# Performance work log

Measured on AMD Instinct MI355X. Metric: run time of the kernel, lower is better.

The kernel has to match this reference:

```python
import jax, jax.numpy as jnp
import numpy as np


def _add_self_loops(src, dst, n):
    loop = jnp.arange(n, dtype=src.dtype)
    return jnp.concatenate([src, loop]), jnp.concatenate([dst, loop])


def _graph_conv(x, src, dst, n, W, b):
    # DGL GraphConv with norm='both':
    #   h = D_in^{-1/2} * A^T * (D_out^{-1/2} * x) @ W + b
    ones = jnp.ones(src.shape, dtype=x.dtype)
    deg_out = jax.ops.segment_sum(ones, src, num_segments=n)
    deg_in = jax.ops.segment_sum(ones, dst, num_segments=n)
    norm_s = jax.lax.rsqrt(jnp.maximum(deg_out, 1.0))
    norm_d = jax.lax.rsqrt(jnp.maximum(deg_in, 1.0))
    msg = (x * norm_s[:, None])[src]                      # [E, d] gather
    agg = jax.ops.segment_sum(msg, dst, num_segments=n)   # [N, d] scatter-add
    return (agg * norm_d[:, None]) @ W + b


def _ntype_forward(x, src, dst, W0, b0, W1, b1):
    n = x.shape[0]
    src, dst = _add_self_loops(src, dst, n)  # dgl.add_self_loop each layer; graph is static
    h = _graph_conv(x, src, dst, n, W0, b0)
    h = jax.nn.relu(h)  # dropout skipped: eval mode (training=False)
    h = _graph_conv(h, src, dst, n, W1, b1)
    return h


def setup_inputs() -> dict:
    key = jax.random.key(0)
    ks = jax.random.split(key, 16)
    NA, NB, EA, EB = 50000, 30000, 600000, 300000
    DA, DB, H = 256, 128, 128
    s = 0.05
    return {
        "feat_a": jax.random.normal(ks[0], (NA, DA), jnp.float32),
        "feat_b": jax.random.normal(ks[1], (NB, DB), jnp.float32),
        "src_a": jax.random.randint(ks[2], (EA,), 0, NA),
        "dst_a": jax.random.randint(ks[3], (EA,), 0, NA),
        "src_b": jax.random.randint(ks[4], (EB,), 0, NB),
        "dst_b": jax.random.randint(ks[5], (EB,), 0, NB),
        "Wa0": jax.random.normal(ks[6], (DA, H), jnp.float32) * s,
        "ba0": jnp.zeros((H,), jnp.float32),
        "Wa1": jax.random.normal(ks[7], (H, H), jnp.float32) * s,
        "ba1": jnp.zeros((H,), jnp.float32),
        "Wb0": jax.random.normal(ks[8], (DB, H), jnp.float32) * s,
        "bb0": jnp.zeros((H,), jnp.float32),
        "Wb1": jax.random.normal(ks[9], (H, H), jnp.float32) * s,
        "bb1": jnp.zeros((H,), jnp.float32),
    }


def reference(feat_a, feat_b, src_a, dst_a, src_b, dst_b,
              Wa0, ba0, Wa1, ba1, Wb0, bb0, Wb1, bb1):
    h_a = _ntype_forward(feat_a, src_a, dst_a, Wa0, ba0, Wa1, ba1)
    h_b = _ntype_forward(feat_b, src_b, dst_b, Wb0, bb0, Wb1, bb1)
    return h_a, h_b
```

## Files before the change

kernel.cpp:

```cpp
#include <hip/hip_runtime.h>
#include <hip/hip_bf16.h>

#define H 128
#define BK 64
#define LDSTR 72

#define EPB 4096
#define BUCK_BITS 8
#define BUCK 256

typedef _Float16 f16;
typedef unsigned int u32;
typedef __attribute__((ext_vector_type(8))) _Float16 f16x8;
typedef __attribute__((ext_vector_type(4))) _Float16 f16x4;
typedef __attribute__((ext_vector_type(4))) float floatx4;

static inline __host__ int ceil_div(int a, int b) { return (a + b - 1) / b; }

__global__ __launch_bounds__(256) void p1K(
    const int* __restrict__ sA, const int* __restrict__ dA, int EA, int nblkA, int nbinsA,
    const int* __restrict__ sB, const int* __restrict__ dB, int EB, int nblkB, int nbinsB,
    int* __restrict__ ch, int offAd, int offBd, int offAs, int offBs, int Lall,
    const float* __restrict__ Wa0, f16* ta0, const float* __restrict__ Wa1, f16* ta1,
    const float* __restrict__ Wb0, f16* tb0, const float* __restrict__ Wb1, f16* tb1, int DA) {
    __shared__ int bd[BUCK], bs[BUCK];
    int bid = blockIdx.x, t = threadIdx.x;
    int p1n = nblkA + nblkB;
    if (bid < p1n) {
        const int *src, *dst; int E, nblk, nbins, blk, od, os;
        if (bid < nblkA) { src = sA; dst = dA; E = EA; nblk = nblkA; nbins = nbinsA; blk = bid; od = offAd; os = offAs; }
        else { src = sB; dst = dB; E = EB; nblk = nblkB; nbins = nbinsB; blk = bid - nblkA; od = offBd; os = offBs; }
        bd[t] = 0; bs[t] = 0;
        __syncthreads();
        int e0 = blk * EPB, e1 = min(E, e0 + EPB);
        for (int e = e0 + t; e < e1; e += 256) {
            atomicAdd(&bd[dst[e] >> BUCK_BITS], 1);
            atomicAdd(&bs[src[e] >> BUCK_BITS], 1);
        }
        __syncthreads();
        for (int b = t; b < nbins; b += 256) {
            ch[od + b * nblk + blk] = bd[b];
            ch[os + b * nblk + blk] = bs[b];
        }
        if (bid == 0 && t == 0) ch[Lall] = 0;
    } else {
        int b2 = bid - p1n;
        int k2 = b2 * 2 + (t >> 7);
        const float* W; f16* T; int D, k;
        if (k2 < DA) { W = Wa0; T = ta0; D = DA; k = k2; }
        else if (k2 < DA + H) { W = Wa1; T = ta1; D = H; k = k2 - DA; }
        else if (k2 < DA + 2 * H) { W = Wb0; T = tb0; D = H; k = k2 - DA - H; }
        else { W = Wb1; T = tb1; D = H; k = k2 - DA - 2 * H; }
        int c = t & 127;
        T[(size_t)c * D + k] = (f16)W[(size_t)k * H + c];
    }
}

__global__ __launch_bounds__(256) void scan1K(int* __restrict__ ch, int n, int* __restrict__ bsum) {
    __shared__ int sh[256];
    int t = threadIdx.x;
    int base = blockIdx.x * 1024 + t * 4;
    int v[4];
#pragma unroll
    for (int i = 0; i < 4; i++) v[i] = (base + i < n) ? ch[base + i] : 0;
    int s = v[0] + v[1] + v[2] + v[3];
    sh[t] = s;
    __syncthreads();
    for (int off = 1; off < 256; off <<= 1) {
        int x = (t >= off) ? sh[t - off] : 0;
        __syncthreads();
        sh[t] += x;
        __syncthreads();
    }
    int run = sh[t] - s;
#pragma unroll
    for (int i = 0; i < 4; i++) {
        if (base + i < n) ch[base + i] = run;
        run += v[i];
    }
    if (t == 255) bsum[blockIdx.x] = sh[255];
}

__global__ void scan2K(int* bsum, int nb) {
    __shared__ int sh[256];
    int t = threadIdx.x;
    int v = (t < nb) ? bsum[t] : 0;
    sh[t] = v;
    __syncthreads();
    for (int off = 1; off < 256; off <<= 1) {
        int x = (t >= off) ? sh[t - off] : 0;
        __syncthreads();
        sh[t] += x;
        __syncthreads();
    }
    if (t < nb) bsum[t] = sh[t] - v;
}

__global__ void scan3K(int* __restrict__ ch, const int* __restrict__ bsum, int n) {
    int i = blockIdx.x * 256 + threadIdx.x;
    if (i < n) ch[i] += bsum[i >> 10];
}

__global__ __launch_bounds__(256) void p3K(
    const int* __restrict__ sA, const int* __restrict__ dA, int EA, int nblkA, int nbinsA,
    const int* __restrict__ sB, const int* __restrict__ dB, int EB, int nblkB, int nbinsB,
    const int* __restrict__ ch, int offAd, int offBd, int offAs, int offBs,
    u32* __restrict__ binned) {
    __shared__ int cd[BUCK], cs[BUCK], ofd[BUCK], ofs[BUCK];
    const int *src, *dst; int E, nblk, nbins, blk, od, os;
    if ((int)blockIdx.x < nblkA) {
        src = sA; dst = dA; E = EA; nblk = nblkA; nbins = nbinsA; blk = blockIdx.x; od = offAd; os = offAs;
    } else {
        src = sB; dst = dB; E = EB; nblk = nblkB; nbins = nbinsB; blk = blockIdx.x - nblkA; od = offBd; os = offBs;
    }
    int t = threadIdx.x;
    cd[t] = 0; cs[t] = 0;
    if (t < nbins) {
        ofd[t] = ch[od + t * nblk + blk];
        ofs[t] = ch[os + t * nblk + blk];
    }
    __syncthreads();
    int e0 = blk * EPB, e1 = min(E, e0 + EPB);
    for (int e = e0 + t; e < e1; e += 256) {
        int d = dst[e], s = src[e];
        int b = d >> BUCK_BITS;
        int r = atomicAdd(&cd[b], 1);
        binned[ofd[b] + r] = (u32)s | ((u32)(d & (BUCK - 1)) << 16);
        int b2 = s >> BUCK_BITS;
        int r2 = atomicAdd(&cs[b2], 1);
        binned[ofs[b2] + r2] = (u32)(s & (BUCK - 1));
    }
}

__global__ __launch_bounds__(256) void p4K(
    const u32* __restrict__ binned, const int* __restrict__ ch,
    int nbinsA, int nblkA, int offAd, int offAs,
    int nbinsB, int nblkB, int offBd, int offBs,
    int* __restrict__ rpA, float* __restrict__ ndA, int* __restrict__ esA, int NA, int EA,
    int* __restrict__ rpB, float* __restrict__ ndB, int* __restrict__ esB, int NB, int EB,
    float* __restrict__ nsA, float* __restrict__ nsB) {
    __shared__ int cnt[BUCK], pos[BUCK], fill[BUCK];
    int bid = blockIdx.x, t = threadIdx.x;
    int ndst = nbinsA + nbinsB;
    if (bid == 0 && t == 0) { rpA[NA] = EA; rpB[NB] = EB; }
    if (bid < ndst) {
        int blk, offm, nblkm, N, ebase; int* rp; float* nd; int* es;
        if (bid < nbinsA) { blk = bid; offm = offAd; nblkm = nblkA; rp = rpA; nd = ndA; es = esA; N = NA; ebase = 0; }
        else { blk = bid - nbinsA; offm = offBd; nblkm = nblkB; rp = rpB; nd = ndB; es = esB; N = NB; ebase = EA; }
        int e0 = ch[offm + blk * nblkm];
        int e1 = ch[offm + (blk + 1) * nblkm];
        cnt[t] = 0; fill[t] = 0;
        __syncthreads();
        for (int e = e0 + t; e < e1; e += 256) atomicAdd(&cnt[(binned[e] >> 16) & 255], 1);
        __syncthreads();
        int c = cnt[t];
        int node = (blk << BUCK_BITS) + t;
        if (node < N) nd[node] = rsqrtf((float)(c + 1));
        pos[t] = c;
        __syncthreads();
        for (int off = 1; off < 256; off <<= 1) {
            int x = (t >= off) ? pos[t - off] : 0;
            __syncthreads();
            pos[t] += x;
            __syncthreads();
        }
        int start = e0 + pos[t] - c - ebase;
        pos[t] = start;
        if (node < N) rp[node] = start;
        __syncthreads();
        for (int e = e0 + t; e < e1; e += 256) {
            u32 w = binned[e];
            int i = (w >> 16) & 255;
            int r = atomicAdd(&fill[i], 1);
            es[pos[i] + r] = (int)(w & 0xFFFFu);
        }
    } else {
        int b2 = bid - ndst;
        int blk, offm, nblkm, N; float* ns;
        if (b2 < nbinsA) { blk = b2; offm = offAs; nblkm = nblkA; ns = nsA; N = NA; }
        else { blk = b2 - nbinsA; offm = offBs; nblkm = nblkB; ns = nsB; N = NB; }
        int e0 = ch[offm + blk * nblkm];
        int e1 = ch[offm + (blk + 1) * nblkm];
        cnt[t] = 0;
        __syncthreads();
        for (int e = e0 + t; e < e1; e += 256) atomicAdd(&cnt[binned[e] & 255], 1);
        __syncthreads();
        int node = (blk << BUCK_BITS) + t;
        if (node < N) ns[node] = rsqrtf((float)(cnt[t] + 1));
    }
}

__global__ __launch_bounds__(256) void gemmF(
    const float* __restrict__ X32A, const f16* __restrict__ X16A, const f16* __restrict__ WtA,
    const float* __restrict__ nsA, f16* __restrict__ YA, int NA, int DA, int nblkA,
    const float* __restrict__ X32B, const f16* __restrict__ X16B, const f16* __restrict__ WtB,
    const float* __restrict__ nsB, f16* __restrict__ YB, int NB, int DB, int xf16) {
    const float* X32; const f16* X16; const f16* Wt; const float* ns; f16* Y; int N, D, bid;
    if ((int)blockIdx.x < nblkA) {
        X32 = X32A; X16 = X16A; Wt = WtA; ns = nsA; Y = YA; N = NA; D = DA; bid = blockIdx.x;
    } else {
        X32 = X32B; X16 = X16B; Wt = WtB; ns = nsB; Y = YB; N = NB; D = DB; bid = blockIdx.x - nblkA;
    }
    __shared__ f16 Xs[64 * LDSTR];
    __shared__ f16 Ws[128 * LDSTR];
    int t = threadIdx.x;
    int wv = t >> 6, lane = t & 63;
    int m = lane & 15, q = lane >> 4;
    int rowbase = bid * 64;

    floatx4 acc[8];
#pragma unroll
    for (int c = 0; c < 8; c++) acc[c] = (floatx4)(0.f);

    for (int k0 = 0; k0 < D; k0 += BK) {
        __syncthreads();
        if (xf16) {
            int kq = (t & 7) * 8;
            int r0 = t >> 3;
#pragma unroll
            for (int i = 0; i < 2; i++) {
                int r = r0 + i * 32;
                int grow = rowbase + r;
                f16x8 v = (f16x8)(f16)0;
                if (grow < N) v = *(const f16x8*)(X16 + (size_t)grow * D + k0 + kq);
                *(f16x8*)&Xs[r * LDSTR + kq] = v;
            }
        } else {
            int kq = (t & 15) * 4;
#pragma unroll
            for (int i = 0; i < 4; i++) {
                int r = (t >> 4) + i * 16;
                int grow = rowbase + r;
                float4 v = make_float4(0.f, 0.f, 0.f, 0.f);
                float nv = 0.f;
                if (grow < N) {
                    v = *(const float4*)(X32 + (size_t)grow * D + k0 + kq);
                    nv = ns[grow];
                }
                f16x4 hv;
                hv[0] = (f16)(v.x * nv); hv[1] = (f16)(v.y * nv);
                hv[2] = (f16)(v.z * nv); hv[3] = (f16)(v.w * nv);
                *(f16x4*)&Xs[r * LDSTR + kq] = hv;
            }
        }
        {
            int ks = (t & 7) * 8;
            int rb = t >> 3;
#pragma unroll
            for (int i = 0; i < 4; i++) {
                int c = rb + i * 32;
                *(f16x8*)&Ws[c * LDSTR + ks] = *(const f16x8*)&Wt[(size_t)c * D + k0 + ks];
            }
        }
        __syncthreads();
#pragma unroll
        for (int ks = 0; ks < BK; ks += 32) {
            f16x8 a = *(const f16x8*)&Xs[(wv * 16 + m) * LDSTR + ks + q * 8];
#pragma unroll
            for (int c = 0; c < 8; c++) {
                f16x8 b = *(const f16x8*)&Ws[(c * 16 + m) * LDSTR + ks + q * 8];
                acc[c] = __builtin_amdgcn_mfma_f32_16x16x32_f16(a, b, acc[c], 0, 0, 0);
            }
        }
    }
#pragma unroll
    for (int c = 0; c < 8; c++)
#pragma unroll
        for (int r = 0; r < 4; r++) {
            int grow = rowbase + wv * 16 + q * 4 + r;
            if (grow < N) Y[(size_t)grow * H + c * 16 + m] = (f16)acc[c][r];
        }
}

__global__ __launch_bounds__(256) void aggC(
    const f16* __restrict__ YA, const int* __restrict__ rpA, const int* __restrict__ esA,
    const float* __restrict__ ndA, const float* __restrict__ nsA, const float* __restrict__ bA,
    float* __restrict__ oA, f16* __restrict__ hA, int nA32, int NA,
    const f16* __restrict__ YB, const int* __restrict__ rpB, const int* __restrict__ esB,
    const float* __restrict__ ndB, const float* __restrict__ nsB, const float* __restrict__ bB,
    float* __restrict__ oB, f16* __restrict__ hB, int NB, int layer0) {
    const f16* Y; const int *rp, *es; const float *nd, *ns, *bias; float* out; f16* hout;
    int N, blk;
    if ((int)blockIdx.x < nA32) {
        Y = YA; rp = rpA; es = esA; nd = ndA; ns = nsA; bias = bA; out = oA; hout = hA;
        N = NA; blk = blockIdx.x;
    } else {
        Y = YB; rp = rpB; es = esB; nd = ndB; ns = nsB; bias = bB; out = oB; hout = hB;
        N = NB; blk = blockIdx.x - nA32;
    }
    int t = threadIdx.x;
    int slot = t >> 3;
    int d = t & 7;
    int node = blk * 32 + slot;
    bool act = node < N;
    int nc = act ? node : (N - 1);
    int beg = rp[nc];
    int cnt = act ? (rp[nc + 1] - beg) : 0;
    int tot = cnt + 1;
    const f16* Yd = Y + (size_t)d * 16;
    float acc[16];
#pragma unroll
    for (int i = 0; i < 16; i++) acc[i] = 0.f;
    int i0 = (0 < cnt) ? es[beg]     : nc;
    int i1 = (1 < cnt) ? es[beg + 1] : nc;
    int i2 = (2 < cnt) ? es[beg + 2] : nc;
    int i3 = (3 < cnt) ? es[beg + 3] : nc;
    int j = 0;
    for (; j + 4 <= tot; j += 4) {
        f16x8 a0 = *(const f16x8*)(Yd + (size_t)i0 * H);
        f16x8 b0 = *(const f16x8*)(Yd + (size_t)i0 * H + 8);
        f16x8 a1 = *(const f16x8*)(Yd + (size_t)i1 * H);
        f16x8 b1 = *(const f16x8*)(Yd + (size_t)i1 * H + 8);
        f16x8 a2 = *(const f16x8*)(Yd + (size_t)i2 * H);
        f16x8 b2 = *(const f16x8*)(Yd + (size_t)i2 * H + 8);
        f16x8 a3 = *(const f16x8*)(Yd + (size_t)i3 * H);
        f16x8 b3 = *(const f16x8*)(Yd + (size_t)i3 * H + 8);
        int jn = j + 4;
        int n0 = (jn     < cnt) ? es[beg + jn]     : nc;
        int n1 = (jn + 1 < cnt) ? es[beg + jn + 1] : nc;
        int n2 = (jn + 2 < cnt) ? es[beg + jn + 2] : nc;
        int n3 = (jn + 3 < cnt) ? es[beg + jn + 3] : nc;
#pragma unroll
        for (int i = 0; i < 8; i++) {
            acc[i]     += ((float)a0[i] + (float)a1[i]) + ((float)a2[i] + (float)a3[i]);
            acc[i + 8] += ((float)b0[i] + (float)b1[i]) + ((float)b2[i] + (float)b3[i]);
        }
        i0 = n0; i1 = n1; i2 = n2; i3 = n3;
    }
    int rem = tot - j;
    if (rem > 0) {
        f16x8 a0 = *(const f16x8*)(Yd + (size_t)i0 * H);
        f16x8 b0 = *(const f16x8*)(Yd + (size_t)i0 * H + 8);
        if (rem > 1) {
            f16x8 a1 = *(const f16x8*)(Yd + (size_t)i1 * H);
            f16x8 b1 = *(const f16x8*)(Yd + (size_t)i1 * H + 8);
            if (rem > 2) {
                f16x8 a2 = *(const f16x8*)(Yd + (size_t)i2 * H);
                f16x8 b2 = *(const f16x8*)(Yd + (size_t)i2 * H + 8);
#pragma unroll
                for (int i = 0; i < 8; i++) {
                    acc[i]     += ((float)a0[i] + (float)a1[i]) + (float)a2[i];
                    acc[i + 8] += ((float)b0[i] + (float)b1[i]) + (float)b2[i];
                }
            } else {
#pragma unroll
                for (int i = 0; i < 8; i++) {
                    acc[i]     += (float)a0[i] + (float)a1[i];
                    acc[i + 8] += (float)b0[i] + (float)b1[i];
                }
            }
        } else {
#pragma unroll
            for (int i = 0; i < 8; i++) {
                acc[i]     += (float)a0[i];
                acc[i + 8] += (float)b0[i];
            }
        }
    }
    if (act) {
        float ndv = nd[node];
        float4 c0 = *(const float4*)(bias + d * 16);
        float4 c1 = *(const float4*)(bias + d * 16 + 4);
        float4 c2 = *(const float4*)(bias + d * 16 + 8);
        float4 c3 = *(const float4*)(bias + d * 16 + 12);
        float o_[16];
        o_[0]  = fmaf(acc[0],  ndv, c0.x); o_[1]  = fmaf(acc[1],  ndv, c0.y);
        o_[2]  = fmaf(acc[2],  ndv, c0.z); o_[3]  = fmaf(acc[3],  ndv, c0.w);
        o_[4]  = fmaf(acc[4],  ndv, c1.x); o_[5]  = fmaf(acc[5],  ndv, c1.y);
        o_[6]  = fmaf(acc[6],  ndv, c1.z); o_[7]  = fmaf(acc[7],  ndv, c1.w);
        o_[8]  = fmaf(acc[8],  ndv, c2.x); o_[9]  = fmaf(acc[9],  ndv, c2.y);
        o_[10] = fmaf(acc[10], ndv, c2.z); o_[11] = fmaf(acc[11], ndv, c2.w);
        o_[12] = fmaf(acc[12], ndv, c3.x); o_[13] = fmaf(acc[13], ndv, c3.y);
        o_[14] = fmaf(acc[14], ndv, c3.z); o_[15] = fmaf(acc[15], ndv, c3.w);
        if (layer0) {
            float nsv = ns[node];
            f16x8 h0, h1;
#pragma unroll
            for (int i = 0; i < 8; i++) {
                h0[i] = (f16)(fmaxf(o_[i], 0.f) * nsv);
                h1[i] = (f16)(fmaxf(o_[i + 8], 0.f) * nsv);
            }
            *(f16x8*)(hout + (size_t)node * H + d * 16) = h0;
            *(f16x8*)(hout + (size_t)node * H + d * 16 + 8) = h1;
        } else {
            float* op = out + (size_t)node * H + d * 16;
            *(float4*)op       = make_float4(o_[0],  o_[1],  o_[2],  o_[3]);
            *(float4*)(op + 4) = make_float4(o_[4],  o_[5],  o_[6],  o_[7]);
            *(float4*)(op + 8) = make_float4(o_[8],  o_[9],  o_[10], o_[11]);
            *(float4*)(op + 12)= make_float4(o_[12], o_[13], o_[14], o_[15]);
        }
    }
}


struct TypeBufs {
    int *rowptr, *esrc;
    float *norm_s, *norm_d;
    f16 *h, *y, *wt0, *wt1;
};

extern "C" void kernel_launch(void* const* d_in, const int* in_sizes, int n_in,
                              void* d_out, int out_size, void* d_ws, size_t ws_size,
                              hipStream_t stream) {
    (void)n_in; (void)out_size; (void)ws_size;
    const float* feat_a = (const float*)d_in[0];
    const float* feat_b = (const float*)d_in[1];
    const int* src_a = (const int*)d_in[2];
    const int* dst_a = (const int*)d_in[3];
    const int* src_b = (const int*)d_in[4];
    const int* dst_b = (const int*)d_in[5];
    const float* Wa0 = (const float*)d_in[6];
    const float* ba0 = (const float*)d_in[7];
    const float* Wa1 = (const float*)d_in[8];
    const float* ba1 = (const float*)d_in[9];
    const float* Wb0 = (const float*)d_in[10];
    const float* bb0 = (const float*)d_in[11];
    const float* Wb1 = (const float*)d_in[12];
    const float* bb1 = (const float*)d_in[13];

    const int DA = in_sizes[6] / H;
    const int DB = in_sizes[10] / H;
    const int NA = in_sizes[0] / DA;
    const int NB = in_sizes[1] / DB;
    const int EA = in_sizes[2];
    const int EB = in_sizes[4];

    const int nblkA = ceil_div(EA, EPB), nblkB = ceil_div(EB, EPB);
    const int nbinsA = ceil_div(NA, BUCK), nbinsB = ceil_div(NB, BUCK);
    const int LAd = nbinsA * nblkA, LBd = nbinsB * nblkB;
    const int offAd = 0;
    const int offBd = LAd;
    const int offAs = offBd + LBd;
    const int offBs = offAs + LAd;
    const int Lall = offBs + LBd;

    char* w = (char*)d_ws;
    auto carve = [&](size_t bytes) {
        void* p = (void*)w;
        w += (bytes + 255) & ~(size_t)255;
        return p;
    };
    int* ch = (int*)carve(((size_t)Lall + 1) * 4);
    int* bsum = (int*)carve(256 * 4);
    u32* binned = (u32*)carve((size_t)2 * (EA + EB) * 4);
    auto carve_type = [&](int N, int E, int D) {
        TypeBufs tb;
        tb.rowptr = (int*)carve(((size_t)N + 1) * 4);
        tb.esrc   = (int*)carve((size_t)E * 4);
        tb.norm_s = (float*)carve((size_t)N * 4);
        tb.norm_d = (float*)carve((size_t)N * 4);
        tb.h      = (f16*)carve((size_t)N * H * 2);
        tb.y      = (f16*)carve((size_t)N * H * 2);
        tb.wt0    = (f16*)carve((size_t)D * H * 2);
        tb.wt1    = (f16*)carve((size_t)H * H * 2);
        return tb;
    };
    TypeBufs A = carve_type(NA, EA, DA);
    TypeBufs B = carve_type(NB, EB, DB);

    float* out_a = (float*)d_out;
    float* out_b = out_a + (size_t)NA * H;

    const int gblkA = ceil_div(NA, 64), gblkB = ceil_div(NB, 64);
    const int nA32 = ceil_div(NA, 32), nB32 = ceil_div(NB, 32);
    const int wcBlocks = (DA + 3 * H) / 2;
    const int nScan = Lall + 1;
    const int sb1 = ceil_div(nScan, 1024);

    p1K<<<nblkA + nblkB + wcBlocks, 256, 0, stream>>>(
        src_a, dst_a, EA, nblkA, nbinsA, src_b, dst_b, EB, nblkB, nbinsB,
        ch, offAd, offBd, offAs, offBs, Lall,
        Wa0, A.wt0, Wa1, A.wt1, Wb0, B.wt0, Wb1, B.wt1, DA);
    scan1K<<<sb1, 256, 0, stream>>>(ch, nScan, bsum);
    scan2K<<<1, 256, 0, stream>>>(bsum, sb1);
    scan3K<<<ceil_div(nScan, 256), 256, 0, stream>>>(ch, bsum, nScan);
    p3K<<<nblkA + nblkB, 256, 0, stream>>>(
        src_a, dst_a, EA, nblkA, nbinsA, src_b, dst_b, EB, nblkB, nbinsB,
        ch, offAd, offBd, offAs, offBs, binned);
    p4K<<<2 * (nbinsA + nbinsB), 256, 0, stream>>>(
        binned, ch, nbinsA, nblkA, offAd, offAs, nbinsB, nblkB, offBd, offBs,
        A.rowptr, A.norm_d, A.esrc, NA, EA,
        B.rowptr, B.norm_d, B.esrc, NB, EB,
        A.norm_s, B.norm_s);
    gemmF<<<gblkA + gblkB, 256, 0, stream>>>(
        feat_a, (const f16*)nullptr, A.wt0, A.norm_s, A.y, NA, DA, gblkA,
        feat_b, (const f16*)nullptr, B.wt0, B.norm_s, B.y, NB, DB, 0);
    aggC<<<nA32 + nB32, 256, 0, stream>>>(
        A.y, A.rowptr, A.esrc, A.norm_d, A.norm_s, ba0, out_a, A.h, nA32, NA,
        B.y, B.rowptr, B.esrc, B.norm_d, B.norm_s, bb0, out_b, B.h, NB, 1);
    gemmF<<<gblkA + gblkB, 256, 0, stream>>>(
        (const float*)nullptr, A.h, A.wt1, A.norm_s, A.y, NA, H, gblkA,
        (const float*)nullptr, B.h, B.wt1, B.norm_s, B.y, NB, H, 1);
    aggC<<<nA32 + nB32, 256, 0, stream>>>(
        A.y, A.rowptr, A.esrc, A.norm_d, A.norm_s, ba1, out_a, A.h, nA32, NA,
        B.y, B.rowptr, B.esrc, B.norm_d, B.norm_s, bb1, out_b, B.h, NB, 0);
}
```

Before: 265.6 us.

## Fuse graph preprocessing kernels into one cooperative kernel with grid syncs

Merges the histogram/weight-transpose, three-stage scan, binning scatter and CSR build kernels into a single cooperatively launched kernel separated by grid-wide barriers. This removes five kernel launches and their inter-kernel gaps on the stream. In exchange, every phase runs at the largest grid size needed by any phase, and each grid barrier has its own cost. The cooperative launch also requires all blocks to be co-resident.

New measurement: 659.2 us. 2.48x slower.

```diff
diff --git a/kernel.cpp b/kernel.cpp
--- a/kernel.cpp
+++ b/kernel.cpp
@@ -1,5 +1,8 @@
 #include <hip/hip_runtime.h>
 #include <hip/hip_bf16.h>
+#include <hip/hip_cooperative_groups.h>
+
+namespace cg = cooperative_groups;
 
 #define H 128
 #define BK 64
@@ -17,176 +20,171 @@
 
 static inline __host__ int ceil_div(int a, int b) { return (a + b - 1) / b; }
 
-__global__ __launch_bounds__(256) void p1K(
-    const int* __restrict__ sA, const int* __restrict__ dA, int EA, int nblkA, int nbinsA,
-    const int* __restrict__ sB, const int* __restrict__ dB, int EB, int nblkB, int nbinsB,
-    int* __restrict__ ch, int offAd, int offBd, int offAs, int offBs, int Lall,
-    const float* __restrict__ Wa0, f16* ta0, const float* __restrict__ Wa1, f16* ta1,
-    const float* __restrict__ Wb0, f16* tb0, const float* __restrict__ Wb1, f16* tb1, int DA) {
-    __shared__ int bd[BUCK], bs[BUCK];
+struct PrepArgs {
+    const int *sA, *dA; int EA, nblkA, nbinsA;
+    const int *sB, *dB; int EB, nblkB, nbinsB;
+    int* ch; int offAd, offBd, offAs, offBs, Lall;
+    const float* Wa0; f16* ta0; const float* Wa1; f16* ta1;
+    const float* Wb0; f16* tb0; const float* Wb1; f16* tb1; int DA;
+    int nScan, sb1; int* bsum;
+    u32* binned;
+    int* rpA; float* ndA; int* esA; int NA;
+    int* rpB; float* ndB; int* esB; int NB;
+    float* nsA; float* nsB;
+    int p1n, wcB, ndst2;
+};
+
+__global__ __launch_bounds__(256) void prepK(PrepArgs a) {
+    cg::grid_group grid = cg::this_grid();
+    __shared__ int sm0[256], sm1[256], sm2[256], sm3[256];
     int bid = blockIdx.x, t = threadIdx.x;
-    int p1n = nblkA + nblkB;
-    if (bid < p1n) {
+
+    if (bid < a.p1n) {
         const int *src, *dst; int E, nblk, nbins, blk, od, os;
-        if (bid < nblkA) { src = sA; dst = dA; E = EA; nblk = nblkA; nbins = nbinsA; blk = bid; od = offAd; os = offAs; }
-        else { src = sB; dst = dB; E = EB; nblk = nblkB; nbins = nbinsB; blk = bid - nblkA; od = offBd; os = offBs; }
-        bd[t] = 0; bs[t] = 0;
+        if (bid < a.nblkA) { src = a.sA; dst = a.dA; E = a.EA; nblk = a.nblkA; nbins = a.nbinsA; blk = bid; od = a.offAd; os = a.offAs; }
+        else { src = a.sB; dst = a.dB; E = a.EB; nblk = a.nblkB; nbins = a.nbinsB; blk = bid - a.nblkA; od = a.offBd; os = a.offBs; }
+        sm0[t] = 0; sm1[t] = 0;
         __syncthreads();
         int e0 = blk * EPB, e1 = min(E, e0 + EPB);
         for (int e = e0 + t; e < e1; e += 256) {
-            atomicAdd(&bd[dst[e] >> BUCK_BITS], 1);
-            atomicAdd(&bs[src[e] >> BUCK_BITS], 1);
+            atomicAdd(&sm0[dst[e] >> BUCK_BITS], 1);
+            atomicAdd(&sm1[src[e] >> BUCK_BITS], 1);
         }
         __syncthreads();
         for (int b = t; b < nbins; b += 256) {
-            ch[od + b * nblk + blk] = bd[b];
-            ch[os + b * nblk + blk] = bs[b];
-        }
-        if (bid == 0 && t == 0) ch[Lall] = 0;
-    } else {
-        int b2 = bid - p1n;
+            a.ch[od + b * nblk + blk] = sm0[b];
+            a.ch[os + b * nblk + blk] = sm1[b];
+        }
+        if (bid == 0 && t == 0) a.ch[a.Lall] = 0;
+    } else if (bid < a.p1n + a.wcB) {
+        int b2 = bid - a.p1n;
         int k2 = b2 * 2 + (t >> 7);
         const float* W; f16* T; int D, k;
-        if (k2 < DA) { W = Wa0; T = ta0; D = DA; k = k2; }
-        else if (k2 < DA + H) { W = Wa1; T = ta1; D = H; k = k2 - DA; }
-        else if (k2 < DA + 2 * H) { W = Wb0; T = tb0; D = H; k = k2 - DA - H; }
-        else { W = Wb1; T = tb1; D = H; k = k2 - DA - 2 * H; }
+        if (k2 < a.DA) { W = a.Wa0; T = a.ta0; D = a.DA; k = k2; }
+        else if (k2 < a.DA + H) { W = a.Wa1; T = a.ta1; D = H; k = k2 - a.DA; }
+        else if (k2 < a.DA + 2 * H) { W = a.Wb0; T = a.tb0; D = H; k = k2 - a.DA - H; }
+        else { W = a.Wb1; T = a.tb1; D = H; k = k2 - a.DA - 2 * H; }
         int c = t & 127;
         T[(size_t)c * D + k] = (f16)W[(size_t)k * H + c];
     }
-}
-
-__global__ __launch_bounds__(256) void scan1K(int* __restrict__ ch, int n, int* __restrict__ bsum) {
-    __shared__ int sh[256];
-    int t = threadIdx.x;
-    int base = blockIdx.x * 1024 + t * 4;
-    int v[4];
-#pragma unroll
-    for (int i = 0; i < 4; i++) v[i] = (base + i < n) ? ch[base + i] : 0;
-    int s = v[0] + v[1] + v[2] + v[3];
-    sh[t] = s;
-    __syncthreads();
-    for (int off = 1; off < 256; off <<= 1) {
-        int x = (t >= off) ? sh[t - off] : 0;
-        __syncthreads();
-        sh[t] += x;
-        __syncthreads();
-    }
-    int run = sh[t] - s;
-#pragma unroll
-    for (int i = 0; i < 4; i++) {
-        if (base + i < n) ch[base + i] = run;
-        run += v[i];
-    }
-    if (t == 255) bsum[blockIdx.x] = sh[255];
-}
-
-__global__ void scan2K(int* bsum, int nb) {
-    __shared__ int sh[256];
-    int t = threadIdx.x;
-    int v = (t < nb) ? bsum[t] : 0;
-    sh[t] = v;
-    __syncthreads();
-    for (int off = 1; off < 256; off <<= 1) {
-        int x = (t >= off) ? sh[t - off] : 0;
-        __syncthreads();
-        sh[t] += x;
-        __syncthreads();
-    }
-    if (t < nb) bsum[t] = sh[t] - v;
-}
-
-__global__ void scan3K(int* __restrict__ ch, const int* __restrict__ bsum, int n) {
-    int i = blockIdx.x * 256 + threadIdx.x;
-    if (i < n) ch[i] += bsum[i >> 10];
-}
-
-__global__ __launch_bounds__(256) void p3K(
-    const int* __restrict__ sA, const int* __restrict__ dA, int EA, int nblkA, int nbinsA,
-    const int* __restrict__ sB, const int* __restrict__ dB, int EB, int nblkB, int nbinsB,
-    const int* __restrict__ ch, int offAd, int offBd, int offAs, int offBs,
-    u32* __restrict__ binned) {
-    __shared__ int cd[BUCK], cs[BUCK], ofd[BUCK], ofs[BUCK];
-    const int *src, *dst; int E, nblk, nbins, blk, od, os;
-    if ((int)blockIdx.x < nblkA) {
-        src = sA; dst = dA; E = EA; nblk = nblkA; nbins = nbinsA; blk = blockIdx.x; od = offAd; os = offAs;
-    } else {
-        src = sB; dst = dB; E = EB; nblk = nblkB; nbins = nbinsB; blk = blockIdx.x - nblkA; od = offBd; os = offBs;
-    }
-    int t = threadIdx.x;
-    cd[t] = 0; cs[t] = 0;
-    if (t < nbins) {
-        ofd[t] = ch[od + t * nblk + blk];
-        ofs[t] = ch[os + t * nblk + blk];
-    }
-    __syncthreads();
-    int e0 = blk * EPB, e1 = min(E, e0 + EPB);
-    for (int e = e0 + t; e < e1; e += 256) {
-        int d = dst[e], s = src[e];
-        int b = d >> BUCK_BITS;
-        int r = atomicAdd(&cd[b], 1);
-        binned[ofd[b] + r] = (u32)s | ((u32)(d & (BUCK - 1)) << 16);
-        int b2 = s >> BUCK_BITS;
-        int r2 = atomicAdd(&cs[b2], 1);
-        binned[ofs[b2] + r2] = (u32)(s & (BUCK - 1));
-    }
-}
-
-__global__ __launch_bounds__(256) void p4K(
-    const u32* __restrict__ binned, const int* __restrict__ ch,
-    int nbinsA, int nblkA, int offAd, int offAs,
-    int nbinsB, int nblkB, int offBd, int offBs,
-    int* __restrict__ rpA, float* __restrict__ ndA, int* __restrict__ esA, int NA, int EA,
-    int* __restrict__ rpB, float* __restrict__ ndB, int* __restrict__ esB, int NB, int EB,
-    float* __restrict__ nsA, float* __restrict__ nsB) {
-    __shared__ int cnt[BUCK], pos[BUCK], fill[BUCK];
-    int bid = blockIdx.x, t = threadIdx.x;
-    int ndst = nbinsA + nbinsB;
-    if (bid == 0 && t == 0) { rpA[NA] = EA; rpB[NB] = EB; }
+    grid.sync();
+
+    if (bid < a.sb1) {
+        int base = bid * 1024 + t * 4;
+        int v[4];
+#pragma unroll
+        for (int i = 0; i < 4; i++) v[i] = (base + i < a.nScan) ? a.ch[base + i] : 0;
+        int s = v[0] + v[1] + v[2] + v[3];
+        sm0[t] = s;
+        __syncthreads();
+        for (int off = 1; off < 256; off <<= 1) {
+            int x = (t >= off) ? sm0[t - off] : 0;
+            __syncthreads();
+            sm0[t] += x;
+            __syncthreads();
+        }
+        int run = sm0[t] - s;
+#pragma unroll
+        for (int i = 0; i < 4; i++) {
+            if (base + i < a.nScan) a.ch[base + i] = run;
+            run += v[i];
+        }
+        if (t == 255) a.bsum[bid] = sm0[255];
+    }
+    grid.sync();
+
+    if (bid == 0) {
+        int v = (t < a.sb1) ? a.bsum[t] : 0;
+        sm0[t] = v;
+        __syncthreads();
+        for (int off = 1; off < 256; off <<= 1) {
+            int x = (t >= off) ? sm0[t - off] : 0;
+            __syncthreads();
+            sm0[t] += x;
+            __syncthreads();
+        }
+        if (t < a.sb1) a.bsum[t] = sm0[t] - v;
+    }
+    grid.sync();
+
+    {
+        int i = bid * 256 + t;
+        if (i < a.nScan) a.ch[i] += a.bsum[i >> 10];
+    }
+    grid.sync();
+
+    if (bid < a.p1n) {
+        const int *src, *dst; int E, nblk, nbins, blk, od, os;
+        if (bid < a.nblkA) {
+            src = a.sA; dst = a.dA; E = a.EA; nblk = a.nblkA; nbins = a.nbinsA; blk = bid; od = a.offAd; os = a.offAs;
+        } else {
+            src = a.sB; dst = a.dB; E = a.EB; nblk = a.nblkB; nbins = a.nbinsB; blk = bid - a.nblkA; od = a.offBd; os = a.offBs;
+        }
+        sm0[t] = 0; sm1[t] = 0;
+        if (t < nbins) {
+            sm2[t] = a.ch[od + t * nblk + blk];
+            sm3[t] = a.ch[os + t * nblk + blk];
+        }
+        __syncthreads();
+        int e0 = blk * EPB, e1 = min(E, e0 + EPB);
+        for (int e = e0 + t; e < e1; e += 256) {
+            int d = dst[e], s = src[e];
+            int b = d >> BUCK_BITS;
+            int r = atomicAdd(&sm0[b], 1);
+            a.binned[sm2[b] + r] = (u32)s | ((u32)(d & (BUCK - 1)) << 16);
+            int b2 = s >> BUCK_BITS;
+            int r2 = atomicAdd(&sm1[b2], 1);
+            a.binned[sm3[b2] + r2] = (u32)(s & (BUCK - 1));
+        }
+    }
+    grid.sync();
+
+    int ndst = a.nbinsA + a.nbinsB;
+    if (bid == 0 && t == 0) { a.rpA[a.NA] = a.EA; a.rpB[a.NB] = a.EB; }
     if (bid < ndst) {
         int blk, offm, nblkm, N, ebase; int* rp; float* nd; int* es;
-        if (bid < nbinsA) { blk = bid; offm = offAd; nblkm = nblkA; rp = rpA; nd = ndA; es = esA; N = NA; ebase = 0; }
-        else { blk = bid - nbinsA; offm = offBd; nblkm = nblkB; rp = rpB; nd = ndB; es = esB; N = NB; ebase = EA; }
-        int e0 = ch[offm + blk * nblkm];
-        int e1 = ch[offm + (blk + 1) * nblkm];
-        cnt[t] = 0; fill[t] = 0;
-        __syncthreads();
-        for (int e = e0 + t; e < e1; e += 256) atomicAdd(&cnt[(binned[e] >> 16) & 255], 1);
-        __syncthreads();
-        int c = cnt[t];
+        if (bid < a.nbinsA) { blk = bid; offm = a.offAd; nblkm = a.nblkA; rp = a.rpA; nd = a.ndA; es = a.esA; N = a.NA; ebase = 0; }
+        else { blk = bid - a.nbinsA; offm = a.offBd; nblkm = a.nblkB; rp = a.rpB; nd = a.ndB; es = a.esB; N = a.NB; ebase = a.EA; }
+        int e0 = a.ch[offm + blk * nblkm];
+        int e1 = a.ch[offm + (blk + 1) * nblkm];
+        sm0[t] = 0; sm2[t] = 0;
+        __syncthreads();
+        for (int e = e0 + t; e < e1; e += 256) atomicAdd(&sm0[(a.binned[e] >> 16) & 255], 1);
+        __syncthreads();
+        int c = sm0[t];
         int node = (blk << BUCK_BITS) + t;
         if (node < N) nd[node] = rsqrtf((float)(c + 1));
-        pos[t] = c;
+        sm1[t] = c;
         __syncthreads();
         for (int off = 1; off < 256; off <<= 1) {
-            int x = (t >= off) ? pos[t - off] : 0;
+            int x = (t >= off) ? sm1[t - off] : 0;
             __syncthreads();
-            pos[t] += x;
+            sm1[t] += x;
             __syncthreads();
         }
-        int start = e0 + pos[t] - c - ebase;
-        pos[t] = start;
+        int start = e0 + sm1[t] - c - ebase;
+        sm1[t] = start;
         if (node < N) rp[node] = start;
         __syncthreads();
         for (int e = e0 + t; e < e1; e += 256) {
-            u32 w = binned[e];
+            u32 w = a.binned[e];
             int i = (w >> 16) & 255;
-            int r = atomicAdd(&fill[i], 1);
-            es[pos[i] + r] = (int)(w & 0xFFFFu);
-        }
-    } else {
+            int r = atomicAdd(&sm2[i], 1);
+            es[sm1[i] + r] = (int)(w & 0xFFFFu);
+        }
+    } else if (bid < a.ndst2) {
         int b2 = bid - ndst;
         int blk, offm, nblkm, N; float* ns;
-        if (b2 < nbinsA) { blk = b2; offm = offAs; nblkm = nblkA; ns = nsA; N = NA; }
-        else { blk = b2 - nbinsA; offm = offBs; nblkm = nblkB; ns = nsB; N = NB; }
-        int e0 = ch[offm + blk * nblkm];
-        int e1 = ch[offm + (blk + 1) * nblkm];
-        cnt[t] = 0;
-        __syncthreads();
-        for (int e = e0 + t; e < e1; e += 256) atomicAdd(&cnt[binned[e] & 255], 1);
+        if (b2 < a.nbinsA) { blk = b2; offm = a.offAs; nblkm = a.nblkA; ns = a.nsA; N = a.NA; }
+        else { blk = b2 - a.nbinsA; offm = a.offBs; nblkm = a.nblkB; ns = a.nsB; N = a.NB; }
+        int e0 = a.ch[offm + blk * nblkm];
+        int e1 = a.ch[offm + (blk + 1) * nblkm];
+        sm0[t] = 0;
+        __syncthreads();
+        for (int e = e0 + t; e < e1; e += 256) atomicAdd(&sm0[a.binned[e] & 255], 1);
         __syncthreads();
         int node = (blk << BUCK_BITS) + t;
-        if (node < N) ns[node] = rsqrtf((float)(cnt[t] + 1));
+        if (node < N) ns[node] = rsqrtf((float)(sm0[t] + 1));
     }
 }
 
@@ -466,22 +464,31 @@
     const int wcBlocks = (DA + 3 * H) / 2;
     const int nScan = Lall + 1;
     const int sb1 = ceil_div(nScan, 1024);
-
-    p1K<<<nblkA + nblkB + wcBlocks, 256, 0, stream>>>(
-        src_a, dst_a, EA, nblkA, nbinsA, src_b, dst_b, EB, nblkB, nbinsB,
-        ch, offAd, offBd, offAs, offBs, Lall,
-        Wa0, A.wt0, Wa1, A.wt1, Wb0, B.wt0, Wb1, B.wt1, DA);
-    scan1K<<<sb1, 256, 0, stream>>>(ch, nScan, bsum);
-    scan2K<<<1, 256, 0, stream>>>(bsum, sb1);
-    scan3K<<<ceil_div(nScan, 256), 256, 0, stream>>>(ch, bsum, nScan);
-    p3K<<<nblkA + nblkB, 256, 0, stream>>>(
-        src_a, dst_a, EA, nblkA, nbinsA, src_b, dst_b, EB, nblkB, nbinsB,
-        ch, offAd, offBd, offAs, offBs, binned);
-    p4K<<<2 * (nbinsA + nbinsB), 256, 0, stream>>>(
-        binned, ch, nbinsA, nblkA, offAd, offAs, nbinsB, nblkB, offBd, offBs,
-        A.rowptr, A.norm_d, A.esrc, NA, EA,
-        B.rowptr, B.norm_d, B.esrc, NB, EB,
-        A.norm_s, B.norm_s);
+    const int p1n = nblkA + nblkB;
+    const int ndst2 = 2 * (nbinsA + nbinsB);
+
+    int nGrid = p1n + wcBlocks;
+    if (ndst2 > nGrid) nGrid = ndst2;
+    int s3b = ceil_div(nScan, 256);
+    if (s3b > nGrid) nGrid = s3b;
+    if (sb1 > nGrid) nGrid = sb1;
+
+    PrepArgs pa;
+    pa.sA = src_a; pa.dA = dst_a; pa.EA = EA; pa.nblkA = nblkA; pa.nbinsA = nbinsA;
+    pa.sB = src_b; pa.dB = dst_b; pa.EB = EB; pa.nblkB = nblkB; pa.nbinsB = nbinsB;
+    pa.ch = ch; pa.offAd = offAd; pa.offBd = offBd; pa.offAs = offAs; pa.offBs = offBs; pa.Lall = Lall;
+    pa.Wa0 = Wa0; pa.ta0 = A.wt0; pa.Wa1 = Wa1; pa.ta1 = A.wt1;
+    pa.Wb0 = Wb0; pa.tb0 = B.wt0; pa.Wb1 = Wb1; pa.tb1 = B.wt1; pa.DA = DA;
+    pa.nScan = nScan; pa.sb1 = sb1; pa.bsum = bsum;
+    pa.binned = binned;
+    pa.rpA = A.rowptr; pa.ndA = A.norm_d; pa.esA = A.esrc; pa.NA = NA;
+    pa.rpB = B.rowptr; pa.ndB = B.norm_d; pa.esB = B.esrc; pa.NB = NB;
+    pa.nsA = A.norm_s; pa.nsB = B.norm_s;
+    pa.p1n = p1n; pa.wcB = wcBlocks; pa.ndst2 = ndst2;
+
+    void* kargs[] = { (void*)&pa };
+    hipLaunchCooperativeKernel((const void*)prepK, dim3(nGrid), dim3(256), kargs, 0, stream);
+
     gemmF<<<gblkA + gblkB, 256, 0, stream>>>(
         feat_a, (const f16*)nullptr, A.wt0, A.norm_s, A.y, NA, DA, gblkA,
         feat_b, (const f16*)nullptr, B.wt0, B.norm_s, B.y, NB, DB, 0);
```
